# Kernel tuning notes

Measured on AMD Instinct MI355X. Metric: run time of the kernel, lower is better.

## Reference

```python
import math
import jax, jax.numpy as jnp
import numpy as np

B, C, S, E = 4, 8, 512, 512
H = 8
HD = E // H
STRIDE = 4
LOCAL_WINDOW = 32


def _sparse_causal_mask(seq_len, stride, window):
    # allowed[i, j]: local causal window (i-window <= j <= i) OR strided (j % stride == 0 and j < i)
    i = jnp.arange(seq_len)[:, None]
    j = jnp.arange(seq_len)[None, :]
    local = (j <= i) & (j >= i - window)
    strided = (j % stride == 0) & (j < i)
    return local | strided  # already subset of causal (j <= i)


def setup_inputs() -> dict:
    key = jax.random.key(0)
    ks = jax.random.split(key, 11)
    xavier = lambda k, fan: jax.random.uniform(k, (E, E), jnp.float32, -1.0, 1.0) * math.sqrt(6.0 / (2 * E))
    return {
        "query": jax.random.normal(ks[0], (B, C, S, E), jnp.float32),
        "key": jax.random.normal(ks[1], (B, C, S, E), jnp.float32),
        "value": jax.random.normal(ks[2], (B, C, S, E), jnp.float32),
        "Wq": xavier(ks[3], E), "bq": jnp.zeros((E,), jnp.float32),
        "Wk": xavier(ks[4], E), "bk": jnp.zeros((E,), jnp.float32),
        "Wv": xavier(ks[5], E), "bv": jnp.zeros((E,), jnp.float32),
        "Wo": xavier(ks[6], E), "bo": jnp.zeros((E,), jnp.float32),
    }


def reference(query, key, value, Wq, bq, Wk, bk, Wv, bv, Wo, bo):
    b, c, s, e = query.shape
    # projections (nn.Linear: x @ W.T + b)
    q = (query @ Wq.T + bq).reshape(b, c, s, H, HD).transpose(0, 3, 1, 2, 4)  # [b,h,c,s,d]
    k = (key @ Wk.T + bk).reshape(b, c, s, H, HD).transpose(0, 3, 1, 2, 4)
    v = (value @ Wv.T + bv).reshape(b, c, s, H, HD).transpose(0, 3, 1, 2, 4)
    scores = jnp.einsum("bhcsd,bhctd->bhcst", q, k) / math.sqrt(HD)  # [b,h,c,s,s]
    allowed = _sparse_causal_mask(s, STRIDE, LOCAL_WINDOW)  # [s,s] bool
    scores = jnp.where(allowed[None, None, None], scores, -jnp.inf)
    attn = jax.nn.softmax(scores, axis=-1)
    context = jnp.einsum("bhcst,bhctd->bhcsd", attn, v)
    context = context.transpose(0, 2, 3, 1, 4).reshape(b, c, s, e)  # [b,c,s,e]
    output = context @ Wo.T + bo
    return output, attn
```

## Files before the change

### kernel.cpp

```cpp
#include <hip/hip_runtime.h>
#include <math.h>

#define Bb 4
#define Cc 8
#define Ss 512
#define Ee 512
#define Hh 8
#define HDd 64
#define LOCALW 32
#define NTOK (Bb*Cc*Ss)
#define RS 40

typedef __attribute__((ext_vector_type(8))) __bf16 bf16x8;
typedef __attribute__((ext_vector_type(4))) float floatx4;
typedef __attribute__((ext_vector_type(4))) unsigned short ushort4v;

__device__ __forceinline__ unsigned short f2bf(float f) {
  union { float f; unsigned int i; } x; x.f = f;
  unsigned int r = x.i + 0x7fffu + ((x.i >> 16) & 1u);
  return (unsigned short)(r >> 16);
}

__device__ __forceinline__ float sexp(float x) { return __expf(fmaxf(x, -80.0f)); }

__global__ __launch_bounds__(256) void cvt3_f32_bf16(
    const float4* __restrict__ s0, const float4* __restrict__ s1, const float4* __restrict__ s2,
    ushort4v* __restrict__ d0, ushort4v* __restrict__ d1, ushort4v* __restrict__ d2, int n4)
{
  const float4* src = (blockIdx.y == 0) ? s0 : (blockIdx.y == 1) ? s1 : s2;
  ushort4v*    dst  = (blockIdx.y == 0) ? d0 : (blockIdx.y == 1) ? d1 : d2;
  int idx = blockIdx.x * blockDim.x + threadIdx.x;
  int stride = gridDim.x * blockDim.x;
  for (int i = idx; i < n4; i += stride) {
    float4 v = src[i];
    ushort4v o;
    o[0] = f2bf(v.x); o[1] = f2bf(v.y); o[2] = f2bf(v.z); o[3] = f2bf(v.w);
    dst[i] = o;
  }
}

__global__ __launch_bounds__(256) void cvtW_f32_bf16(
    const float4* __restrict__ s0, const float4* __restrict__ s1,
    const float4* __restrict__ s2, const float4* __restrict__ s3,
    ushort4v* __restrict__ d0, ushort4v* __restrict__ d1,
    ushort4v* __restrict__ d2, ushort4v* __restrict__ d3, int n4)
{
  const float4* src = (blockIdx.y == 0) ? s0 : (blockIdx.y == 1) ? s1 : (blockIdx.y == 2) ? s2 : s3;
  ushort4v*    dst  = (blockIdx.y == 0) ? d0 : (blockIdx.y == 1) ? d1 : (blockIdx.y == 2) ? d2 : d3;
  int idx = blockIdx.x * blockDim.x + threadIdx.x;
  int stride = gridDim.x * blockDim.x;
  for (int i = idx; i < n4; i += stride) {
    float4 v = src[i];
    ushort4v o;
    o[0] = f2bf(v.x); o[1] = f2bf(v.y); o[2] = f2bf(v.z); o[3] = f2bf(v.w);
    dst[i] = o;
  }
}

#define NXB (Ee/128)
#define NYB (NTOK/128)
template <bool F32OUT>
__global__ __launch_bounds__(256, 2) void gemm_nt_bias3(
    const unsigned short* __restrict__ X0, const unsigned short* __restrict__ X1,
    const unsigned short* __restrict__ X2,
    const unsigned short* __restrict__ W0, const unsigned short* __restrict__ W1,
    const unsigned short* __restrict__ W2,
    const float* __restrict__ bias0, const float* __restrict__ bias1,
    const float* __restrict__ bias2,
    void* __restrict__ out0, void* __restrict__ out1, void* __restrict__ out2)
{
  const int z = blockIdx.z;
  const unsigned short* X = (z == 0) ? X0 : (z == 1) ? X1 : X2;
  const unsigned short* W = (z == 0) ? W0 : (z == 1) ? W1 : W2;
  const float* bias        = (z == 0) ? bias0 : (z == 1) ? bias1 : bias2;
  void* outv               = (z == 0) ? out0 : (z == 1) ? out1 : out2;

  __shared__ unsigned short As[2][128 * 64];
  __shared__ unsigned short Bs[2][128 * 64];

  const int id   = blockIdx.x + NXB * blockIdx.y;
  const int orig = (id & 7) * (NXB * NYB / 8) + (id >> 3);
  const int m_blk = (orig >> 2) * 128;
  const int n_blk = (orig & (NXB - 1)) * 128;

  const int K = Ee, N = Ee;
  const int lane = threadIdx.x & 63;
  const int wave = threadIdx.x >> 6;
  const int r16  = lane & 15;
  const int oct  = lane >> 4;
  const int wm = (wave >> 1) * 64;
  const int wn = (wave & 1) * 64;

  const int row8  = lane >> 3;
  const int chSrc = (lane & 7) ^ row8;

  floatx4 acc[4][4];
  #pragma unroll
  for (int a = 0; a < 4; ++a)
    #pragma unroll
    for (int b = 0; b < 4; ++b)
      acc[a][b] = (floatx4)(0.0f);

  #pragma unroll
  for (int t = 0; t < 4; ++t) {
    const int rbase = t * 32 + wave * 8;
    __builtin_amdgcn_global_load_lds(
        (const __attribute__((address_space(1))) unsigned int*)(X + (size_t)(m_blk + rbase + row8) * K + chSrc * 8),
        (__attribute__((address_space(3))) unsigned int*)(As[0] + rbase * 64), 16, 0, 0);
    __builtin_amdgcn_global_load_lds(
        (const __attribute__((address_space(1))) unsigned int*)(W + (size_t)(n_blk + rbase + row8) * K + chSrc * 8),
        (__attribute__((address_space(3))) unsigned int*)(Bs[0] + rbase * 64), 16, 0, 0);
  }
  __syncthreads();

  #pragma unroll
  for (int kt = 0; kt < 8; ++kt) {
    const int cur = kt & 1;
    if (kt < 7) {
      const int kb = (kt + 1) * 64;
      #pragma unroll
      for (int t = 0; t < 4; ++t) {
        const int rbase = t * 32 + wave * 8;
        __builtin_amdgcn_global_load_lds(
            (const __attribute__((address_space(1))) unsigned int*)(X + (size_t)(m_blk + rbase + row8) * K + kb + chSrc * 8),
            (__attribute__((address_space(3))) unsigned int*)(As[cur ^ 1] + rbase * 64), 16, 0, 0);
        __builtin_amdgcn_global_load_lds(
            (const __attribute__((address_space(1))) unsigned int*)(W + (size_t)(n_blk + rbase + row8) * K + kb + chSrc * 8),
            (__attribute__((address_space(3))) unsigned int*)(Bs[cur ^ 1] + rbase * 64), 16, 0, 0);
      }
    }

    #pragma unroll
    for (int s = 0; s < 2; ++s) {
      bf16x8 af[4], bfq[4];
      #pragma unroll
      for (int mi = 0; mi < 4; ++mi) {
        const int row = wm + mi * 16 + r16;
        af[mi] = *(const bf16x8*)(As[cur] + row * 64 + ((s * 4 + oct) ^ (r16 & 7)) * 8);
      }
      #pragma unroll
      for (int ni = 0; ni < 4; ++ni) {
        const int row = wn + ni * 16 + r16;
        bfq[ni] = *(const bf16x8*)(Bs[cur] + row * 64 + ((s * 4 + oct) ^ (r16 & 7)) * 8);
      }
      #pragma unroll
      for (int mi = 0; mi < 4; ++mi)
        #pragma unroll
        for (int ni = 0; ni < 4; ++ni)
          acc[mi][ni] = __builtin_amdgcn_mfma_f32_16x16x32_bf16(af[mi], bfq[ni], acc[mi][ni], 0, 0, 0);
    }
    __syncthreads();
  }

  float bv[4];
  #pragma unroll
  for (int ni = 0; ni < 4; ++ni) bv[ni] = bias[n_blk + wn + ni * 16 + r16];

  #pragma unroll
  for (int mi = 0; mi < 4; ++mi)
    #pragma unroll
    for (int ni = 0; ni < 4; ++ni)
      #pragma unroll
      for (int r = 0; r < 4; ++r) {
        const int m = m_blk + wm + mi * 16 + oct * 4 + r;
        const int n = n_blk + wn + ni * 16 + r16;
        const float val = acc[mi][ni][r] + bv[ni];
        if (F32OUT) __builtin_nontemporal_store(val, (float*)outv + (size_t)m * N + n);
        else        ((unsigned short*)outv)[(size_t)m * N + n] = f2bf(val);
      }
}

__global__ __launch_bounds__(512, 4) void attn_kernel(
    const unsigned short* __restrict__ Q,
    const unsigned short* __restrict__ Kb,
    const unsigned short* __restrict__ V,
    float* __restrict__ attn_out,
    unsigned short* __restrict__ ctx)
{
  __shared__ unsigned short VT[HDd][Ss];
  __shared__ unsigned short scr[8][16 * RS];

  const int slice = blockIdx.x;
  const int c  = slice & (Cc - 1);
  const int bh = slice >> 3;
  const int h  = bh & (Hh - 1);
  const int b  = bh >> 3;
  const size_t tokBase  = (size_t)(b * Cc + c) * Ss;
  const size_t attnBase = (size_t)slice * Ss * Ss;

  const int tid  = threadIdx.x;
  const int lane = tid & 63;
  const int wave = tid >> 6;
  const int r16  = lane & 15;
  const int oct  = lane >> 4;
  unsigned short* sw = scr[wave];

  {
    const int d0 = wave * 8;
    const unsigned short* vbase = V + tokBase * Ee + h * HDd + d0;
    #pragma unroll
    for (int pass = 0; pass < 4; ++pass) {
      const int j0 = pass * 128 + lane * 2;
      const uint4 ra = *(const uint4*)(vbase + (size_t)j0 * Ee);
      const uint4 rb = *(const uint4*)(vbase + (size_t)(j0 + 1) * Ee);
      const unsigned int aw[4] = {ra.x, ra.y, ra.z, ra.w};
      const unsigned int bw[4] = {rb.x, rb.y, rb.z, rb.w};
      #pragma unroll
      for (int k = 0; k < 8; ++k) {
        const unsigned int av = (k & 1) ? (aw[k >> 1] >> 16) : (aw[k >> 1] & 0xffffu);
        const unsigned int bv = (k & 1) ? (bw[k >> 1] >> 16) : (bw[k >> 1] & 0xffffu);
        *(unsigned int*)(&VT[d0 + k][j0 ^ (k << 3)]) = av | (bv << 16);
      }
    }
  }
  __syncthreads();

  const int rt0 = 2 * wave + blockIdx.y;
  for (int t = 0; t < 2; ++t) {
    const int rt = t ? (31 - rt0) : rt0;
    const int I  = rt * 16;
    const int i  = I + r16;

    const unsigned short* qrow = Q + (tokBase + i) * Ee + h * HDd + oct * 8;
    const bf16x8 qa0 = *(const bf16x8*)(qrow);
    const bf16x8 qa1 = *(const bf16x8*)(qrow + 32);
    const unsigned short* kbase = Kb + (tokBase + r16) * Ee + h * HDd + oct * 8;
    const int ij0 = i - 4 * oct;

    float m_a = -INFINITY, l_a = 0.0f, m_b = -INFINITY, l_b = 0.0f;
    const int farEnd = rt - 2;
    int ct = 0;
    for (; ct + 1 < farEnd; ct += 2) {
      const unsigned short* kr0 = kbase + (size_t)ct * (16 * Ee);
      const unsigned short* kr1 = kbase + (size_t)(ct + 1) * (16 * Ee);
      const bf16x8 ka0 = *(const bf16x8*)(kr0);
      const bf16x8 ka1 = *(const bf16x8*)(kr0 + 32);
      const bf16x8 kc0 = *(const bf16x8*)(kr1);
      const bf16x8 kc1 = *(const bf16x8*)(kr1 + 32);
      floatx4 a = (floatx4)(0.0f), a2 = (floatx4)(0.0f);
      a  = __builtin_amdgcn_mfma_f32_16x16x32_bf16(ka0, qa0, a, 0, 0, 0);
      a  = __builtin_amdgcn_mfma_f32_16x16x32_bf16(ka1, qa1, a, 0, 0, 0);
      a2 = __builtin_amdgcn_mfma_f32_16x16x32_bf16(kc0, qa0, a2, 0, 0, 0);
      a2 = __builtin_amdgcn_mfma_f32_16x16x32_bf16(kc1, qa1, a2, 0, 0, 0);
      const float v0 = a[0] * 0.125f;
      const float w0 = a2[0] * 0.125f;
      float mn = fmaxf(m_a, v0);
      l_a = l_a * sexp(m_a - mn) + sexp(v0 - mn);
      m_a = mn;
      mn = fmaxf(m_b, w0);
      l_b = l_b * sexp(m_b - mn) + sexp(w0 - mn);
      m_b = mn;
    }
    for (; ct < farEnd; ++ct) {
      const unsigned short* krow = kbase + (size_t)ct * (16 * Ee);
      const bf16x8 kb0 = *(const bf16x8*)(krow);
      const bf16x8 kb1 = *(const bf16x8*)(krow + 32);
      floatx4 a = (floatx4)(0.0f);
      a = __builtin_amdgcn_mfma_f32_16x16x32_bf16(kb0, qa0, a, 0, 0, 0);
      a = __builtin_amdgcn_mfma_f32_16x16x32_bf16(kb1, qa1, a, 0, 0, 0);
      const float v0 = a[0] * 0.125f;
      const float mn = fmaxf(m_a, v0);
      l_a = l_a * sexp(m_a - mn) + sexp(v0 - mn);
      m_a = mn;
    }
    for (ct = (farEnd > 0 ? farEnd : 0); ct <= rt; ++ct) {
      const unsigned short* krow = kbase + (size_t)ct * (16 * Ee);
      const bf16x8 kb0 = *(const bf16x8*)(krow);
      const bf16x8 kb1 = *(const bf16x8*)(krow + 32);
      floatx4 a = (floatx4)(0.0f);
      a = __builtin_amdgcn_mfma_f32_16x16x32_bf16(kb0, qa0, a, 0, 0, 0);
      a = __builtin_amdgcn_mfma_f32_16x16x32_bf16(kb1, qa1, a, 0, 0, 0);
      const int dib = ij0 - 16 * ct;
      const float v0 = (dib >= 0)                   ? a[0] * 0.125f : -INFINITY;
      const float v1 = ((unsigned)(dib - 1) <= 32u) ? a[1] * 0.125f : -INFINITY;
      const float v2 = ((unsigned)(dib - 2) <= 32u) ? a[2] * 0.125f : -INFINITY;
      const float v3 = ((unsigned)(dib - 3) <= 32u) ? a[3] * 0.125f : -INFINITY;
      const float mx4 = fmaxf(fmaxf(v0, v1), fmaxf(v2, v3));
      const float mn = fmaxf(m_a, mx4);
      l_a = l_a * sexp(m_a - mn)
          + sexp(v0 - mn) + sexp(v1 - mn) + sexp(v2 - mn) + sexp(v3 - mn);
      m_a = mn;
    }
    float m = fmaxf(m_a, m_b);
    float l = l_a * sexp(m_a - m) + l_b * sexp(m_b - m);
    #pragma unroll
    for (int msk = 16; msk <= 32; msk <<= 1) {
      const float mo = __shfl_xor(m, msk, 64);
      const float lo = __shfl_xor(l, msk, 64);
      const float mn = fmaxf(m, mo);
      l = l * sexp(m - mn) + lo * sexp(mo - mn);
      m = mn;
    }
    const float cc = -m - __logf(l);

    const int jcMax = rt >> 1;
    floatx4 cacc[4];
    #pragma unroll
    for (int dt = 0; dt < 4; ++dt) cacc[dt] = (floatx4)(0.0f);
    float* attnRow = attn_out + attnBase + (size_t)i * Ss + oct * 4;
    unsigned short* swrow = sw + r16 * RS;

    for (int jc = 0; jc <= jcMax; ++jc) {
      #pragma unroll
      for (int h2 = 0; h2 < 2; ++h2) {
        const int ctp = 2 * jc + h2;
        float p0 = 0.0f, p1 = 0.0f, p2 = 0.0f, p3 = 0.0f;
        if (ctp <= rt) {
          const unsigned short* krow = kbase + (size_t)ctp * (16 * Ee);
          const bf16x8 kb0 = *(const bf16x8*)(krow);
          const bf16x8 kb1 = *(const bf16x8*)(krow + 32);
          floatx4 a = (floatx4)(0.0f);
          a = __builtin_amdgcn_mfma_f32_16x16x32_bf16(kb0, qa0, a, 0, 0, 0);
          a = __builtin_amdgcn_mfma_f32_16x16x32_bf16(kb1, qa1, a, 0, 0, 0);
          if (ctp < farEnd) {
            p0 = __expf(a[0] * 0.125f + cc);
          } else {
            const int dib = ij0 - 16 * ctp;
            if (dib >= 0)                   p0 = __expf(a[0] * 0.125f + cc);
            if ((unsigned)(dib - 1) <= 32u) p1 = __expf(a[1] * 0.125f + cc);
            if ((unsigned)(dib - 2) <= 32u) p2 = __expf(a[2] * 0.125f + cc);
            if ((unsigned)(dib - 3) <= 32u) p3 = __expf(a[3] * 0.125f + cc);
          }
        }
        __builtin_nontemporal_store((floatx4){p0, p1, p2, p3},
                                    (floatx4*)(attnRow + (size_t)ctp * 16));
        const unsigned int plo = (unsigned int)f2bf(p0) | ((unsigned int)f2bf(p1) << 16);
        const unsigned int phi = (unsigned int)f2bf(p2) | ((unsigned int)f2bf(p3) << 16);
        *(uint2*)(swrow + h2 * 16 + oct * 4) = make_uint2(plo, phi);
      }
      const bf16x8 pa = *(const bf16x8*)(swrow + oct * 8);
      #pragma unroll
      for (int dt = 0; dt < 4; ++dt) {
        const int d = dt * 16 + r16;
        const bf16x8 vb = *(const bf16x8*)(&VT[d][(jc * 32 + oct * 8) ^ ((d & 7) << 3)]);
        cacc[dt] = __builtin_amdgcn_mfma_f32_16x16x32_bf16(vb, pa, cacc[dt], 0, 0, 0);
      }
    }
    const floatx4 z4 = (floatx4)(0.0f);
    for (int ctz = 2 * (jcMax + 1); ctz < 32; ++ctz)
      __builtin_nontemporal_store(z4, (floatx4*)(attnRow + (size_t)ctz * 16));
    #pragma unroll
    for (int dt = 0; dt < 4; ++dt) {
      const unsigned int lo = (unsigned int)f2bf(cacc[dt][0]) | ((unsigned int)f2bf(cacc[dt][1]) << 16);
      const unsigned int hi = (unsigned int)f2bf(cacc[dt][2]) | ((unsigned int)f2bf(cacc[dt][3]) << 16);
      *(uint2*)(ctx + (tokBase + i) * Ee + h * HDd + dt * 16 + oct * 4) = make_uint2(lo, hi);
    }
  }
}

extern "C" void kernel_launch(void* const* d_in, const int* in_sizes, int n_in,
                              void* d_out, int out_size, void* d_ws, size_t ws_size,
                              hipStream_t stream) {
  const float* query = (const float*)d_in[0];
  const float* key_  = (const float*)d_in[1];
  const float* value = (const float*)d_in[2];
  const float* Wq = (const float*)d_in[3];
  const float* bq = (const float*)d_in[4];
  const float* Wk = (const float*)d_in[5];
  const float* bk = (const float*)d_in[6];
  const float* Wv = (const float*)d_in[7];
  const float* bv = (const float*)d_in[8];
  const float* Wo = (const float*)d_in[9];
  const float* bo = (const float*)d_in[10];

  float* out  = (float*)d_out;
  float* attn = out + (size_t)Bb*Cc*Ss*Ee;

  unsigned short* ws = (unsigned short*)d_ws;
  unsigned short* qb  = ws;
  unsigned short* kb  = qb  + (size_t)NTOK * Ee;
  unsigned short* vb  = kb  + (size_t)NTOK * Ee;
  unsigned short* Qw  = vb  + (size_t)NTOK * Ee;
  unsigned short* Kw  = Qw  + (size_t)NTOK * Ee;
  unsigned short* Vw  = Kw  + (size_t)NTOK * Ee;
  unsigned short* Cw  = Vw  + (size_t)NTOK * Ee;
  unsigned short* Wqb = Cw  + (size_t)NTOK * Ee;
  unsigned short* Wkb = Wqb + (size_t)Ee * Ee;
  unsigned short* Wvb = Wkb + (size_t)Ee * Ee;
  unsigned short* Wob = Wvb + (size_t)Ee * Ee;

  const int n4big = NTOK * Ee / 4;
  const int n4w   = Ee * Ee / 4;
  cvt3_f32_bf16<<<dim3(1024, 3), 256, 0, stream>>>(
      (const float4*)query, (const float4*)key_, (const float4*)value,
      (ushort4v*)qb, (ushort4v*)kb, (ushort4v*)vb, n4big);
  cvtW_f32_bf16<<<dim3(128, 4), 256, 0, stream>>>(
      (const float4*)Wq, (const float4*)Wk, (const float4*)Wv, (const float4*)Wo,
      (ushort4v*)Wqb, (ushort4v*)Wkb, (ushort4v*)Wvb, (ushort4v*)Wob, n4w);

  dim3 blk(256);
  gemm_nt_bias3<false><<<dim3(NXB, NYB, 3), blk, 0, stream>>>(
      qb, kb, vb, Wqb, Wkb, Wvb, bq, bk, bv, Qw, Kw, Vw);

  attn_kernel<<<dim3(Bb*Hh*Cc, 2), 512, 0, stream>>>(Qw, Kw, Vw, attn, Cw);

  gemm_nt_bias3<true><<<dim3(NXB, NYB, 1), blk, 0, stream>>>(
      Cw, Cw, Cw, Wob, Wob, Wob, bo, bo, bo, out, out, out);
}
```

Measured before the change: 484.7 us.

## Fuse fp32-to-bf16 conversion into projection GEMM tile loads

```diff
diff --git a/kernel.cpp b/kernel.cpp
--- a/kernel.cpp
+++ b/kernel.cpp
@@ -13,7 +13,7 @@
 
 typedef __attribute__((ext_vector_type(8))) __bf16 bf16x8;
 typedef __attribute__((ext_vector_type(4))) float floatx4;
-typedef __attribute__((ext_vector_type(4))) unsigned short ushort4v;
+typedef __attribute__((ext_vector_type(8))) unsigned short ushort8v;
 
 __device__ __forceinline__ unsigned short f2bf(float f) {
   union { float f; unsigned int i; } x; x.f = f;
@@ -23,57 +23,28 @@
 
 __device__ __forceinline__ float sexp(float x) { return __expf(fmaxf(x, -80.0f)); }
 
-__global__ __launch_bounds__(256) void cvt3_f32_bf16(
-    const float4* __restrict__ s0, const float4* __restrict__ s1, const float4* __restrict__ s2,
-    ushort4v* __restrict__ d0, ushort4v* __restrict__ d1, ushort4v* __restrict__ d2, int n4)
-{
-  const float4* src = (blockIdx.y == 0) ? s0 : (blockIdx.y == 1) ? s1 : s2;
-  ushort4v*    dst  = (blockIdx.y == 0) ? d0 : (blockIdx.y == 1) ? d1 : d2;
-  int idx = blockIdx.x * blockDim.x + threadIdx.x;
-  int stride = gridDim.x * blockDim.x;
-  for (int i = idx; i < n4; i += stride) {
-    float4 v = src[i];
-    ushort4v o;
-    o[0] = f2bf(v.x); o[1] = f2bf(v.y); o[2] = f2bf(v.z); o[3] = f2bf(v.w);
-    dst[i] = o;
-  }
-}
-
-__global__ __launch_bounds__(256) void cvtW_f32_bf16(
-    const float4* __restrict__ s0, const float4* __restrict__ s1,
-    const float4* __restrict__ s2, const float4* __restrict__ s3,
-    ushort4v* __restrict__ d0, ushort4v* __restrict__ d1,
-    ushort4v* __restrict__ d2, ushort4v* __restrict__ d3, int n4)
-{
-  const float4* src = (blockIdx.y == 0) ? s0 : (blockIdx.y == 1) ? s1 : (blockIdx.y == 2) ? s2 : s3;
-  ushort4v*    dst  = (blockIdx.y == 0) ? d0 : (blockIdx.y == 1) ? d1 : (blockIdx.y == 2) ? d2 : d3;
-  int idx = blockIdx.x * blockDim.x + threadIdx.x;
-  int stride = gridDim.x * blockDim.x;
-  for (int i = idx; i < n4; i += stride) {
-    float4 v = src[i];
-    ushort4v o;
-    o[0] = f2bf(v.x); o[1] = f2bf(v.y); o[2] = f2bf(v.z); o[3] = f2bf(v.w);
-    dst[i] = o;
-  }
+__device__ __forceinline__ void cvt_write8(unsigned short* dst, const float4 a, const float4 b) {
+  ushort8v o;
+  o[0] = f2bf(a.x); o[1] = f2bf(a.y); o[2] = f2bf(a.z); o[3] = f2bf(a.w);
+  o[4] = f2bf(b.x); o[5] = f2bf(b.y); o[6] = f2bf(b.z); o[7] = f2bf(b.w);
+  *(ushort8v*)dst = o;
 }
 
 #define NXB (Ee/128)
 #define NYB (NTOK/128)
-template <bool F32OUT>
-__global__ __launch_bounds__(256, 2) void gemm_nt_bias3(
-    const unsigned short* __restrict__ X0, const unsigned short* __restrict__ X1,
-    const unsigned short* __restrict__ X2,
-    const unsigned short* __restrict__ W0, const unsigned short* __restrict__ W1,
-    const unsigned short* __restrict__ W2,
+template <bool XBF16, bool F32OUT>
+__global__ __launch_bounds__(256, 2) void gemm_cvt_bias3(
+    const void* __restrict__ X0v, const void* __restrict__ X1v, const void* __restrict__ X2v,
+    const float* __restrict__ W0, const float* __restrict__ W1, const float* __restrict__ W2,
     const float* __restrict__ bias0, const float* __restrict__ bias1,
     const float* __restrict__ bias2,
     void* __restrict__ out0, void* __restrict__ out1, void* __restrict__ out2)
 {
   const int z = blockIdx.z;
-  const unsigned short* X = (z == 0) ? X0 : (z == 1) ? X1 : X2;
-  const unsigned short* W = (z == 0) ? W0 : (z == 1) ? W1 : W2;
-  const float* bias        = (z == 0) ? bias0 : (z == 1) ? bias1 : bias2;
-  void* outv               = (z == 0) ? out0 : (z == 1) ? out1 : out2;
+  const void*  Xv   = (z == 0) ? X0v : (z == 1) ? X1v : X2v;
+  const float* Wf   = (z == 0) ? W0  : (z == 1) ? W1  : W2;
+  const float* bias = (z == 0) ? bias0 : (z == 1) ? bias1 : bias2;
+  void* outv        = (z == 0) ? out0 : (z == 1) ? out1 : out2;
 
   __shared__ unsigned short As[2][128 * 64];
   __shared__ unsigned short Bs[2][128 * 64];
@@ -84,15 +55,23 @@
   const int n_blk = (orig & (NXB - 1)) * 128;
 
   const int K = Ee, N = Ee;
-  const int lane = threadIdx.x & 63;
-  const int wave = threadIdx.x >> 6;
+  const int tid  = threadIdx.x;
+  const int lane = tid & 63;
+  const int wave = tid >> 6;
   const int r16  = lane & 15;
   const int oct  = lane >> 4;
   const int wm = (wave >> 1) * 64;
   const int wn = (wave & 1) * 64;
 
+  const int rw0  = tid >> 3;
+  const int c8   = tid & 7;
+  const int cPos = c8 ^ (rw0 & 7);
+  const float* Wbase = Wf + (size_t)(n_blk + rw0) * K + c8 * 8;
+  const float* Xfbase = (const float*)Xv + (size_t)(m_blk + rw0) * K + c8 * 8;
+
   const int row8  = lane >> 3;
   const int chSrc = (lane & 7) ^ row8;
+  const unsigned short* Xbf = (const unsigned short*)Xv;
 
   floatx4 acc[4][4];
   #pragma unroll
@@ -101,32 +80,65 @@
     for (int b = 0; b < 4; ++b)
       acc[a][b] = (floatx4)(0.0f);
 
+  float4 ra[4][2], rb[4][2];
+
+  if (!XBF16) {
+    #pragma unroll
+    for (int q = 0; q < 4; ++q) {
+      const float* p = Xfbase + (size_t)(32 * q) * K;
+      ra[q][0] = *(const float4*)(p);
+      ra[q][1] = *(const float4*)(p + 4);
+    }
+  } else {
+    #pragma unroll
+    for (int t = 0; t < 4; ++t) {
+      const int rbase = t * 32 + wave * 8;
+      __builtin_amdgcn_global_load_lds(
+          (const __attribute__((address_space(1))) unsigned int*)(Xbf + (size_t)(m_blk + rbase + row8) * K + chSrc * 8),
+          (__attribute__((address_space(3))) unsigned int*)(As[0] + rbase * 64), 16, 0, 0);
+    }
+  }
   #pragma unroll
-  for (int t = 0; t < 4; ++t) {
-    const int rbase = t * 32 + wave * 8;
-    __builtin_amdgcn_global_load_lds(
-        (const __attribute__((address_space(1))) unsigned int*)(X + (size_t)(m_blk + rbase + row8) * K + chSrc * 8),
-        (__attribute__((address_space(3))) unsigned int*)(As[0] + rbase * 64), 16, 0, 0);
-    __builtin_amdgcn_global_load_lds(
-        (const __attribute__((address_space(1))) unsigned int*)(W + (size_t)(n_blk + rbase + row8) * K + chSrc * 8),
-        (__attribute__((address_space(3))) unsigned int*)(Bs[0] + rbase * 64), 16, 0, 0);
-  }
+  for (int q = 0; q < 4; ++q) {
+    const float* p = Wbase + (size_t)(32 * q) * K;
+    rb[q][0] = *(const float4*)(p);
+    rb[q][1] = *(const float4*)(p + 4);
+  }
+  if (!XBF16) {
+    #pragma unroll
+    for (int q = 0; q < 4; ++q)
+      cvt_write8(As[0] + (rw0 + 32 * q) * 64 + cPos * 8, ra[q][0], ra[q][1]);
+  }
+  #pragma unroll
+  for (int q = 0; q < 4; ++q)
+    cvt_write8(Bs[0] + (rw0 + 32 * q) * 64 + cPos * 8, rb[q][0], rb[q][1]);
   __syncthreads();
 
-  #pragma unroll
   for (int kt = 0; kt < 8; ++kt) {
     const int cur = kt & 1;
     if (kt < 7) {
       const int kb = (kt + 1) * 64;
-      #pragma unroll
-      for (int t = 0; t < 4; ++t) {
-        const int rbase = t * 32 + wave * 8;
-        __builtin_amdgcn_global_load_lds(
-            (const __attribute__((address_space(1))) unsigned int*)(X + (size_t)(m_blk + rbase + row8) * K + kb + chSrc * 8),
-            (__attribute__((address_space(3))) unsigned int*)(As[cur ^ 1] + rbase * 64), 16, 0, 0);
-        __builtin_amdgcn_global_load_lds(
-            (const __attribute__((address_space(1))) unsigned int*)(W + (size_t)(n_blk + rbase + row8) * K + kb + chSrc * 8),
-            (__attribute__((address_space(3))) unsigned int*)(Bs[cur ^ 1] + rbase * 64), 16, 0, 0);
+      if (!XBF16) {
+        #pragma unroll
+        for (int q = 0; q < 4; ++q) {
+          const float* p = Xfbase + (size_t)(32 * q) * K + kb;
+          ra[q][0] = *(const float4*)(p);
+          ra[q][1] = *(const float4*)(p + 4);
+        }
+      } else {
+        #pragma unroll
+        for (int t = 0; t < 4; ++t) {
+          const int rbase = t * 32 + wave * 8;
+          __builtin_amdgcn_global_load_lds(
+              (const __attribute__((address_space(1))) unsigned int*)(Xbf + (size_t)(m_blk + rbase + row8) * K + kb + chSrc * 8),
+              (__attribute__((address_space(3))) unsigned int*)(As[cur ^ 1] + rbase * 64), 16, 0, 0);
+        }
+      }
+      #pragma unroll
+      for (int q = 0; q < 4; ++q) {
+        const float* p = Wbase + (size_t)(32 * q) * K + kb;
+        rb[q][0] = *(const float4*)(p);
+        rb[q][1] = *(const float4*)(p + 4);
       }
     }
 
@@ -148,6 +160,17 @@
         #pragma unroll
         for (int ni = 0; ni < 4; ++ni)
           acc[mi][ni] = __builtin_amdgcn_mfma_f32_16x16x32_bf16(af[mi], bfq[ni], acc[mi][ni], 0, 0, 0);
+    }
+
+    if (kt < 7) {
+      if (!XBF16) {
+        #pragma unroll
+        for (int q = 0; q < 4; ++q)
+          cvt_write8(As[cur ^ 1] + (rw0 + 32 * q) * 64 + cPos * 8, ra[q][0], ra[q][1]);
+      }
+      #pragma unroll
+      for (int q = 0; q < 4; ++q)
+        cvt_write8(Bs[cur ^ 1] + (rw0 + 32 * q) * 64 + cPos * 8, rb[q][0], rb[q][1]);
     }
     __syncthreads();
   }
@@ -367,33 +390,17 @@
   float* attn = out + (size_t)Bb*Cc*Ss*Ee;
 
   unsigned short* ws = (unsigned short*)d_ws;
-  unsigned short* qb  = ws;
-  unsigned short* kb  = qb  + (size_t)NTOK * Ee;
-  unsigned short* vb  = kb  + (size_t)NTOK * Ee;
-  unsigned short* Qw  = vb  + (size_t)NTOK * Ee;
-  unsigned short* Kw  = Qw  + (size_t)NTOK * Ee;
-  unsigned short* Vw  = Kw  + (size_t)NTOK * Ee;
-  unsigned short* Cw  = Vw  + (size_t)NTOK * Ee;
-  unsigned short* Wqb = Cw  + (size_t)NTOK * Ee;
-  unsigned short* Wkb = Wqb + (size_t)Ee * Ee;
-  unsigned short* Wvb = Wkb + (size_t)Ee * Ee;
-  unsigned short* Wob = Wvb + (size_t)Ee * Ee;
-
-  const int n4big = NTOK * Ee / 4;
-  const int n4w   = Ee * Ee / 4;
-  cvt3_f32_bf16<<<dim3(1024, 3), 256, 0, stream>>>(
-      (const float4*)query, (const float4*)key_, (const float4*)value,
-      (ushort4v*)qb, (ushort4v*)kb, (ushort4v*)vb, n4big);
-  cvtW_f32_bf16<<<dim3(128, 4), 256, 0, stream>>>(
-      (const float4*)Wq, (const float4*)Wk, (const float4*)Wv, (const float4*)Wo,
-      (ushort4v*)Wqb, (ushort4v*)Wkb, (ushort4v*)Wvb, (ushort4v*)Wob, n4w);
+  unsigned short* Qw = ws;
+  unsigned short* Kw = Qw + (size_t)NTOK * Ee;
+  unsigned short* Vw = Kw + (size_t)NTOK * Ee;
+  unsigned short* Cw = Vw + (size_t)NTOK * Ee;
 
   dim3 blk(256);
-  gemm_nt_bias3<false><<<dim3(NXB, NYB, 3), blk, 0, stream>>>(
-      qb, kb, vb, Wqb, Wkb, Wvb, bq, bk, bv, Qw, Kw, Vw);
+  gemm_cvt_bias3<false, false><<<dim3(NXB, NYB, 3), blk, 0, stream>>>(
+      query, key_, value, Wq, Wk, Wv, bq, bk, bv, Qw, Kw, Vw);
 
   attn_kernel<<<dim3(Bb*Hh*Cc, 2), 512, 0, stream>>>(Qw, Kw, Vw, attn, Cw);
 
-  gemm_nt_bias3<true><<<dim3(NXB, NYB, 1), blk, 0, stream>>>(
-      Cw, Cw, Cw, Wob, Wob, Wob, bo, bo, bo, out, out, out);
+  gemm_cvt_bias3<true, true><<<dim3(NXB, NYB, 1), blk, 0, stream>>>(
+      Cw, Cw, Cw, Wo, Wo, Wo, bo, bo, bo, out, out, out);
 }
```

Result: slower. 511.1 us (+5.5%).
